# Optimization experiments

Hardware: AMD Instinct MI355X
Metric: run time of the kernel (lower is better)

Reference implementation:

```python
import jax, jax.numpy as jnp
import numpy as np

B, L, D, N_ORIG, GD, K_TARGET = 8, 512, 1024, 8192, 64, 256
_PI, _PJ = np.triu_indices(L, k=1)  # all global pairs i<j, shared across batch


def setup_inputs() -> dict:
    key = jax.random.key(0)
    k1, k2, k3 = jax.random.split(key, 3)
    x = jax.random.normal(k1, (B, L, D), jnp.float32)
    source = jax.random.uniform(k2, (B, L, N_ORIG), jnp.float32)
    W = jax.random.normal(k3, (GD, D), jnp.float32) * 0.02  # group_proj weight (out,in), no bias
    return {"x": x, "source": source, "W": W, "target_len": K_TARGET}


def _merge_single(x, s, W, r_step, pi, pj):
    # x: (S,D), s: (S,N). One greedy global merge step (r_step = S//2 >= r_total).
    S = x.shape[0]
    g = x @ W.T                                   # (S, GD)
    gn = jnp.linalg.norm(g, axis=-1)              # token weights (g.norm)
    gu = g / jnp.maximum(gn, 1e-12)[:, None]      # F.normalize(g, dim=-1)
    sim = (gu[pi] * gu[pj]).sum(-1)               # (P,) cosine sim of each pair
    # deterministic order: (-sim, i, j); lexsort's last key is primary
    order = jnp.lexsort((pj, pi, -sim))
    si = pi[order]
    sj = pj[order]

    # sequential greedy disjoint (mutual-exclusion) selection
    def body(carry, ij):
        partner, isj, cnt = carry
        i, j = ij
        used_i = (partner[i] >= 0) | isj[i]
        used_j = (partner[j] >= 0) | isj[j]
        sel = (~used_i) & (~used_j) & (cnt < r_step)
        partner = partner.at[i].set(jnp.where(sel, j, partner[i]))
        isj = isj.at[j].set(isj[j] | sel)
        return (partner, isj, cnt + sel.astype(jnp.int32)), None

    init = (jnp.full((S,), -1, jnp.int32), jnp.zeros((S,), bool), jnp.int32(0))
    (partner, isj, _), _ = jax.lax.scan(body, init, (si, sj))

    # kept tokens (everything not a merged-away j), in original order; greedy on a
    # complete graph always selects exactly r_step pairs, so K = S - r_step is static
    K = S - r_step
    keep = jnp.argsort(isj.astype(jnp.int32), stable=True)[:K]  # (K,)
    pk = partner[keep]
    has_p = pk >= 0
    pjx = jnp.where(has_p, pk, keep)  # safe partner index
    wi = gn[keep]
    wj = gn[pjx]
    tot = wi + wj + 1e-8
    xm = jnp.where(has_p[:, None], (wi[:, None] * x[keep] + wj[:, None] * x[pjx]) / tot[:, None], x[keep])
    sm = jnp.where(has_p[:, None], s[keep] + s[pjx], s[keep])
    return xm, sm


def reference(x, source, W, target_len):
    Bb, Ll, Dd = x.shape
    r_total = Ll - target_len
    if r_total <= 0:
        return x, source
    # with target_len = L//2, r_total <= floor(L/2): single greedy step (faithful)
    r_step = min(r_total, Ll // 2)
    pi = jnp.asarray(_PI, jnp.int32)
    pj = jnp.asarray(_PJ, jnp.int32)
    f = lambda xb, sb: _merge_single(xb, sb, W, r_step, pi, pj)
    return jax.vmap(f)(x, source)
```

## Files before the change

kernel.cpp:

```cpp
#include <hip/hip_runtime.h>

#define B_ 8
#define L_ 512
#define D_ 1024
#define N_ 8192
#define GD_ 64
#define K_ 256
#define CD_ 24

#define XQ(q) ((q) ^ (((q) >> 4) & 7))

__global__ __launch_bounds__(256) void wt_kernel(const float* __restrict__ W,
                                                 float* __restrict__ Wt) {
  int idx = blockIdx.x * 256 + threadIdx.x;
  int d = idx >> 6, g = idx & 63;
  Wt[idx] = W[(size_t)g * D_ + d];
}

__global__ __launch_bounds__(256) void gproj_kernel(const float* __restrict__ x,
                                                    const float* __restrict__ Wt,
                                                    float* __restrict__ gu,
                                                    float* __restrict__ gn) {
  __shared__ __align__(16) float xs[16 * 1024];
  __shared__ __align__(16) float red[16][16][64];
  int blk = blockIdx.x;
  int b = blk >> 5;
  int t0 = (blk & 31) * 16;
  int tid = threadIdx.x;
  const float* xb = x + ((size_t)b * L_ + t0) * D_;
  for (int r = 0; r < 16; ++r) {
    int idx = r * 256 + tid;
    int tok = idx >> 8, q = idx & 255;
    float4 v = *(const float4*)(xb + (size_t)tok * D_ + q * 4);
    *(float4*)&xs[tok * 1024 + XQ(q) * 4] = v;
  }
  __syncthreads();
  int dq = tid & 15, kg = tid >> 4;
  float acc[16][4];
#pragma unroll
  for (int t = 0; t < 16; ++t)
#pragma unroll
    for (int d = 0; d < 4; ++d) acc[t][d] = 0.f;
  const float* wbase = Wt + (size_t)(kg * 64) * GD_ + dq * 4;
#pragma unroll 1
  for (int sub = 0; sub < 4; ++sub) {
    float4 wv[16];
#pragma unroll
    for (int kk = 0; kk < 16; ++kk)
      wv[kk] = *(const float4*)(wbase + (size_t)(sub * 16 + kk) * GD_);
#pragma unroll
    for (int tok = 0; tok < 16; ++tok) {
      float4 xv[4];
#pragma unroll
      for (int kq = 0; kq < 4; ++kq) {
        int q = kg * 16 + sub * 4 + kq;
        xv[kq] = *(const float4*)&xs[tok * 1024 + XQ(q) * 4];
      }
#pragma unroll
      for (int kq = 0; kq < 4; ++kq) {
        float xc[4] = {xv[kq].x, xv[kq].y, xv[kq].z, xv[kq].w};
#pragma unroll
        for (int c = 0; c < 4; ++c) {
          float4 w = wv[kq * 4 + c];
          acc[tok][0] += xc[c] * w.x;
          acc[tok][1] += xc[c] * w.y;
          acc[tok][2] += xc[c] * w.z;
          acc[tok][3] += xc[c] * w.w;
        }
      }
    }
  }
#pragma unroll
  for (int tok = 0; tok < 16; ++tok) {
    float4 p;
    p.x = acc[tok][0]; p.y = acc[tok][1]; p.z = acc[tok][2]; p.w = acc[tok][3];
    *(float4*)&red[kg][tok][dq * 4] = p;
  }
  __syncthreads();
  int tok = tid >> 4, dqo = tid & 15;
  float g[4] = {0.f, 0.f, 0.f, 0.f};
#pragma unroll
  for (int k = 0; k < 16; ++k) {
    float4 p = *(const float4*)&red[k][tok][dqo * 4];
    g[0] += p.x; g[1] += p.y; g[2] += p.z; g[3] += p.w;
  }
  double ss = 0.0;
#pragma unroll
  for (int d = 0; d < 4; ++d) ss += (double)g[d] * (double)g[d];
#pragma unroll
  for (int off = 1; off < 16; off <<= 1) ss += __shfl_xor(ss, off);
  float gnv = (float)sqrt(ss);
  float dn = fmaxf(gnv, 1e-12f);
  int t = t0 + tok;
  if (dqo == 0) gn[(size_t)b * L_ + t] = gnv;
  float4 o;
  o.x = g[0] / dn; o.y = g[1] / dn; o.z = g[2] / dn; o.w = g[3] / dn;
  *(float4*)(gu + ((size_t)b * L_ + t) * GD_ + dqo * 4) = o;
}

__global__ __launch_bounds__(256) void sim_topk_kernel(const float* __restrict__ gu,
                                                       float* __restrict__ simo,
                                                       unsigned long long* __restrict__ cand) {
  __shared__ __align__(16) float simL[16][512];
  __shared__ __align__(16) float BsT[64][68];
  int b = blockIdx.y;
  int i0 = blockIdx.x * 16;
  const float* gb = gu + (size_t)b * L_ * GD_;
  int tid = threadIdx.x;
  int r = tid >> 4, c4 = (tid & 15) * 4;
  float af[GD_];
  const float4* arow = (const float4*)(gb + (size_t)(i0 + r) * GD_);
#pragma unroll
  for (int q = 0; q < 16; ++q) *(float4*)&af[q * 4] = arow[q];
  float* sgl = simo + (size_t)b * L_ * L_;
#pragma unroll 1
  for (int jt = 0; jt < 8; ++jt) {
    int j0 = jt * 64;
    for (int f = tid; f < 64 * GD_; f += 256) {
      int br = f >> 6, k = f & 63;
      BsT[k][br] = gb[(size_t)(j0 + br) * GD_ + k];
    }
    __syncthreads();
    double a0 = 0, a1 = 0, a2 = 0, a3 = 0;
#pragma unroll
    for (int k = 0; k < GD_; ++k) {
      double a = (double)af[k];
      float4 bv = *(const float4*)&BsT[k][c4];
      a0 += a * (double)bv.x;
      a1 += a * (double)bv.y;
      a2 += a * (double)bv.z;
      a3 += a * (double)bv.w;
    }
    float4 o;
    o.x = (float)a0; o.y = (float)a1; o.z = (float)a2; o.w = (float)a3;
    *(float4*)&simL[r][j0 + c4] = o;
    *(float4*)(sgl + (size_t)(i0 + r) * L_ + (j0 + c4)) = o;
    __syncthreads();
  }
  int wave = tid >> 6, lane = tid & 63;
  for (int rr = wave; rr < 16; rr += 4) {
    int a = i0 + rr;
    int c0 = lane * 8;
    float vv[8];
#pragma unroll
    for (int s = 0; s < 8; ++s) vv[s] = simL[rr][c0 + s];
    unsigned long long k[8];
#pragma unroll
    for (int s = 0; s < 8; ++s) {
      int bb = c0 + s;
      if (bb == a) {
        k[s] = 0;
      } else {
        unsigned u = __float_as_uint(vv[s]);
        u = (u & 0x80000000u) ? ~u : (u | 0x80000000u);
        int i = a < bb ? a : bb, j = a < bb ? bb : a;
        k[s] = ((unsigned long long)u << 18) |
               (unsigned long long)(0x3FFFFu - (((unsigned)i << 9) | (unsigned)j));
      }
    }
    unsigned long long* out = cand + ((size_t)b * L_ + a) * CD_;
#pragma unroll 1
    for (int pass = 0; pass < CD_; ++pass) {
      unsigned long long m = k[0];
#pragma unroll
      for (int s = 1; s < 8; ++s) m = k[s] > m ? k[s] : m;
#pragma unroll
      for (int off = 32; off; off >>= 1) {
        unsigned long long o = __shfl_xor(m, off);
        if (o > m) m = o;
      }
#pragma unroll
      for (int s = 0; s < 8; ++s)
        if (k[s] == m) k[s] = 0;
      if (lane == 0) out[pass] = m;
    }
  }
}

__global__ __launch_bounds__(512) void match_kernel(const float* __restrict__ sim,
                                                    const unsigned long long* __restrict__ cand,
                                                    int* __restrict__ keepI,
                                                    int* __restrict__ keepJ) {
  int b = blockIdx.x;
  const float* S = sim + (size_t)b * L_ * L_;
  const unsigned long long* C = cand + (size_t)b * L_ * CD_;
  __shared__ unsigned long long candL[L_][CD_];
  __shared__ unsigned long long bestkey[L_];
  __shared__ short partner[L_];
  __shared__ short liveA[L_], liveB[L_], rescanQ[L_];
  __shared__ unsigned char liveF[L_], needs[L_], head[L_];
  __shared__ int cnt[2], nQ[2];
  int tid = threadIdx.x;
  int wave = tid >> 6, lane = tid & 63;
  for (int f = tid; f < L_ * (CD_ / 2); f += 512)
    ((ulonglong2*)candL)[f] = ((const ulonglong2*)C)[f];
  if (tid < L_) {
    partner[tid] = -1;
    liveF[tid] = 1;
    needs[tid] = 1;
    head[tid] = 0;
    liveA[tid] = (short)tid;
    bestkey[tid] = 0ull;
  }
  if (tid == 0) {
    cnt[0] = L_; cnt[1] = 0;
    nQ[0] = 0; nQ[1] = 0;
  }
  __syncthreads();
  for (int round = 0; round < 300; ++round) {
    int par = round & 1;
    int nLive = cnt[par];
    if (nLive == 0) break;
    short* cur = par ? liveB : liveA;
    short* nxt = par ? liveA : liveB;
    if (tid == 0) {
      cnt[par ^ 1] = 0;
      nQ[par ^ 1] = 0;
    }
    for (int idx = tid; idx < nLive; idx += 512) {
      int a = cur[idx];
      if (needs[a]) {
        int h = head[a];
        unsigned long long bk = 0ull;
        while (h < CD_) {
          unsigned long long key = candL[a][h];
          if (key) {
            unsigned pk = 0x3FFFFu - (unsigned)(key & 0x3FFFFull);
            int i = (int)(pk >> 9), j = (int)(pk & 511u);
            int p = (i == a) ? j : i;
            if (liveF[p]) { bk = key; break; }
          }
          ++h;
        }
        head[a] = (unsigned char)h;
        if (bk) {
          bestkey[a] = bk;
          needs[a] = 0;
        } else {
          int q = atomicAdd(&nQ[par], 1);
          rescanQ[q] = (short)a;
        }
      }
    }
    __syncthreads();
    int nq = nQ[par];
    if (nq > 0) {
      for (int q = wave; q < nq; q += 8) {
        int a = rescanQ[q];
        unsigned long long mk = 0ull;
        for (int kk = lane; kk < nLive; kk += 64) {
          int bb = cur[kk];
          if (bb != a) {
            float sv = S[(size_t)a * L_ + bb];
            unsigned u = __float_as_uint(sv);
            u = (u & 0x80000000u) ? ~u : (u | 0x80000000u);
            int i = a < bb ? a : bb, j = a < bb ? bb : a;
            unsigned long long key =
                ((unsigned long long)u << 18) |
                (unsigned long long)(0x3FFFFu - (((unsigned)i << 9) | (unsigned)j));
            if (key > mk) mk = key;
          }
        }
#pragma unroll
        for (int off = 32; off; off >>= 1) {
          unsigned long long o = __shfl_xor(mk, off);
          if (o > mk) mk = o;
        }
        if (lane == 0) {
          bestkey[a] = mk;
          needs[a] = 0;
        }
      }
      __syncthreads();
    }
    for (int idx = tid; idx < nLive; idx += 512) {
      int a = cur[idx];
      unsigned pk = 0x3FFFFu - (unsigned)(bestkey[a] & 0x3FFFFull);
      int i = (int)(pk >> 9), j = (int)(pk & 511u);
      int p = (i == a) ? j : i;
      unsigned pk2 = 0x3FFFFu - (unsigned)(bestkey[p] & 0x3FFFFull);
      int i2 = (int)(pk2 >> 9), j2 = (int)(pk2 & 511u);
      int p2 = (i2 == p) ? j2 : i2;
      if (p2 == a) {
        partner[a] = (short)p;
        liveF[a] = 0;
      }
    }
    __syncthreads();
    for (int idx = tid; idx < nLive; idx += 512) {
      int a = cur[idx];
      if (liveF[a]) {
        unsigned pk = 0x3FFFFu - (unsigned)(bestkey[a] & 0x3FFFFull);
        int i = (int)(pk >> 9), j = (int)(pk & 511u);
        int p = (i == a) ? j : i;
        if (!liveF[p]) needs[a] = 1;
        int pos = atomicAdd(&cnt[par ^ 1], 1);
        nxt[pos] = (short)a;
      }
    }
    __syncthreads();
  }
  if (wave == 0) {
    int base = 0;
    for (int c = 0; c < 8; ++c) {
      int a = c * 64 + lane;
      bool kept = partner[a] > a;
      unsigned long long m = __ballot(kept);
      int pos = base + (int)__popcll(m & ((1ull << lane) - 1ull));
      if (kept) {
        keepI[b * K_ + pos] = a;
        keepJ[b * K_ + pos] = partner[a];
      }
      base += (int)__popcll(m);
    }
  }
}

__global__ __launch_bounds__(256) void merge_kernel(const float* __restrict__ x,
                                                    const float* __restrict__ s,
                                                    const float* __restrict__ gn,
                                                    const int* __restrict__ keepI,
                                                    const int* __restrict__ keepJ,
                                                    float* __restrict__ xm,
                                                    float* __restrict__ sm) {
  int blk = blockIdx.x;
  int row = blk >> 1, half = blk & 1;
  int b = row >> 8;
  int i = keepI[row], j = keepJ[row];
  int t = threadIdx.x;
  if (half == 0) {
    float wi = gn[(size_t)b * L_ + i], wj = gn[(size_t)b * L_ + j];
    float tot = wi + wj + 1e-8f;
    const float4* xi = (const float4*)(x + ((size_t)b * L_ + i) * D_);
    const float4* xj = (const float4*)(x + ((size_t)b * L_ + j) * D_);
    float4* o = (float4*)(xm + (size_t)row * D_);
    float4 a = xi[t], c = xj[t];
    float4 r;
    r.x = (wi * a.x + wj * c.x) / tot;
    r.y = (wi * a.y + wj * c.y) / tot;
    r.z = (wi * a.z + wj * c.z) / tot;
    r.w = (wi * a.w + wj * c.w) / tot;
    o[t] = r;
  }
  {
    size_t off = (size_t)half * (N_ / 2);
    const float4* si = (const float4*)(s + ((size_t)b * L_ + i) * N_ + off);
    const float4* sj = (const float4*)(s + ((size_t)b * L_ + j) * N_ + off);
    float4* o = (float4*)(sm + (size_t)row * N_ + off);
    for (int tt = t; tt < N_ / 8; tt += 256) {
      float4 a = si[tt], c = sj[tt];
      float4 r;
      r.x = a.x + c.x;
      r.y = a.y + c.y;
      r.z = a.z + c.z;
      r.w = a.w + c.w;
      o[tt] = r;
    }
  }
}

extern "C" void kernel_launch(void* const* d_in, const int* in_sizes, int n_in,
                              void* d_out, int out_size, void* d_ws, size_t ws_size,
                              hipStream_t stream) {
  (void)in_sizes; (void)n_in; (void)out_size; (void)ws_size;
  const float* x = (const float*)d_in[0];
  const float* src = (const float*)d_in[1];
  const float* W = (const float*)d_in[2];

  float* ws = (float*)d_ws;
  float* Wt = ws;
  float* gu = Wt + 65536;
  float* gn = gu + (size_t)B_ * L_ * GD_;
  float* sim = gn + (size_t)B_ * L_;
  int* keepI = (int*)(sim + (size_t)B_ * L_ * L_);
  int* keepJ = keepI + B_ * K_;
  unsigned long long* cand = (unsigned long long*)(keepJ + B_ * K_);

  float* xm = (float*)d_out;
  float* sm = xm + (size_t)B_ * K_ * D_;

  wt_kernel<<<256, 256, 0, stream>>>(W, Wt);
  gproj_kernel<<<256, 256, 0, stream>>>(x, Wt, gu, gn);
  sim_topk_kernel<<<dim3(32, 8), 256, 0, stream>>>(gu, sim, cand);
  match_kernel<<<B_, 512, 0, stream>>>(sim, cand, keepI, keepJ);
  merge_kernel<<<B_ * K_ * 2, 256, 0, stream>>>(x, src, gn, keepI, keepJ, xm, sm);
}
```

Before: 358.8 us.

## Split sim/top-k into separate tiled kernels and shrink candidate depth

Splits the fused similarity and top-k kernel into a 2D-tiled sim kernel (2048 blocks of 32x32 tiles) and a separate top-k kernel with one wave per row. The fused version ran only 256 blocks, each looping serially over column tiles. The change also cuts the per-row candidate count from 24 to 16, which shortens the top-k passes and shrinks the candidate list the match kernel loads. The split adds an extra launch and a re-read of the sim matrix from global memory. The smaller candidate depth may also make the match kernel fall back to rescans more often.

```diff
diff --git a/kernel.cpp b/kernel.cpp
--- a/kernel.cpp
+++ b/kernel.cpp
@@ -6,7 +6,7 @@
 #define N_ 8192
 #define GD_ 64
 #define K_ 256
-#define CD_ 24
+#define CD_ 16
 
 #define XQ(q) ((q) ^ (((q) >> 4) & 7))
 
@@ -98,82 +98,78 @@
   *(float4*)(gu + ((size_t)b * L_ + t) * GD_ + dqo * 4) = o;
 }
 
-__global__ __launch_bounds__(256) void sim_topk_kernel(const float* __restrict__ gu,
-                                                       float* __restrict__ simo,
-                                                       unsigned long long* __restrict__ cand) {
-  __shared__ __align__(16) float simL[16][512];
-  __shared__ __align__(16) float BsT[64][68];
-  int b = blockIdx.y;
-  int i0 = blockIdx.x * 16;
+__global__ __launch_bounds__(256) void sim_kernel(const float* __restrict__ gu,
+                                                  float* __restrict__ simo) {
+  __shared__ __align__(16) float BsT[GD_][36];
+  int b = blockIdx.z;
+  int i0 = blockIdx.y * 32, j0 = blockIdx.x * 32;
   const float* gb = gu + (size_t)b * L_ * GD_;
   int tid = threadIdx.x;
-  int r = tid >> 4, c4 = (tid & 15) * 4;
+  for (int f = tid; f < 32 * GD_; f += 256) {
+    int r = f >> 6, k = f & 63;
+    BsT[k][r] = gb[(size_t)(j0 + r) * GD_ + k];
+  }
+  int r = tid >> 3, c4 = (tid & 7) * 4;
   float af[GD_];
   const float4* arow = (const float4*)(gb + (size_t)(i0 + r) * GD_);
 #pragma unroll
   for (int q = 0; q < 16; ++q) *(float4*)&af[q * 4] = arow[q];
-  float* sgl = simo + (size_t)b * L_ * L_;
-#pragma unroll 1
-  for (int jt = 0; jt < 8; ++jt) {
-    int j0 = jt * 64;
-    for (int f = tid; f < 64 * GD_; f += 256) {
-      int br = f >> 6, k = f & 63;
-      BsT[k][br] = gb[(size_t)(j0 + br) * GD_ + k];
-    }
-    __syncthreads();
-    double a0 = 0, a1 = 0, a2 = 0, a3 = 0;
-#pragma unroll
-    for (int k = 0; k < GD_; ++k) {
-      double a = (double)af[k];
-      float4 bv = *(const float4*)&BsT[k][c4];
-      a0 += a * (double)bv.x;
-      a1 += a * (double)bv.y;
-      a2 += a * (double)bv.z;
-      a3 += a * (double)bv.w;
-    }
-    float4 o;
-    o.x = (float)a0; o.y = (float)a1; o.z = (float)a2; o.w = (float)a3;
-    *(float4*)&simL[r][j0 + c4] = o;
-    *(float4*)(sgl + (size_t)(i0 + r) * L_ + (j0 + c4)) = o;
-    __syncthreads();
-  }
-  int wave = tid >> 6, lane = tid & 63;
-  for (int rr = wave; rr < 16; rr += 4) {
-    int a = i0 + rr;
-    int c0 = lane * 8;
-    float vv[8];
-#pragma unroll
-    for (int s = 0; s < 8; ++s) vv[s] = simL[rr][c0 + s];
-    unsigned long long k[8];
-#pragma unroll
-    for (int s = 0; s < 8; ++s) {
-      int bb = c0 + s;
-      if (bb == a) {
-        k[s] = 0;
-      } else {
-        unsigned u = __float_as_uint(vv[s]);
-        u = (u & 0x80000000u) ? ~u : (u | 0x80000000u);
-        int i = a < bb ? a : bb, j = a < bb ? bb : a;
-        k[s] = ((unsigned long long)u << 18) |
-               (unsigned long long)(0x3FFFFu - (((unsigned)i << 9) | (unsigned)j));
-      }
-    }
-    unsigned long long* out = cand + ((size_t)b * L_ + a) * CD_;
-#pragma unroll 1
-    for (int pass = 0; pass < CD_; ++pass) {
-      unsigned long long m = k[0];
-#pragma unroll
-      for (int s = 1; s < 8; ++s) m = k[s] > m ? k[s] : m;
-#pragma unroll
-      for (int off = 32; off; off >>= 1) {
-        unsigned long long o = __shfl_xor(m, off);
-        if (o > m) m = o;
-      }
-#pragma unroll
-      for (int s = 0; s < 8; ++s)
-        if (k[s] == m) k[s] = 0;
-      if (lane == 0) out[pass] = m;
-    }
+  __syncthreads();
+  double a0 = 0, a1 = 0, a2 = 0, a3 = 0;
+#pragma unroll
+  for (int k = 0; k < GD_; ++k) {
+    double a = (double)af[k];
+    float4 bv = *(const float4*)&BsT[k][c4];
+    a0 += a * (double)bv.x;
+    a1 += a * (double)bv.y;
+    a2 += a * (double)bv.z;
+    a3 += a * (double)bv.w;
+  }
+  float4 o;
+  o.x = (float)a0; o.y = (float)a1; o.z = (float)a2; o.w = (float)a3;
+  *(float4*)(simo + (size_t)b * L_ * L_ + (size_t)(i0 + r) * L_ + (j0 + c4)) = o;
+}
+
+__global__ __launch_bounds__(256) void topk_kernel(const float* __restrict__ sim,
+                                                   unsigned long long* __restrict__ cand) {
+  int wid = blockIdx.x * 4 + (threadIdx.x >> 6);
+  int b = wid >> 9;
+  int a = wid & 511;
+  int lane = threadIdx.x & 63;
+  const float* row = sim + ((size_t)b * L_ + a) * L_;
+  int c0 = lane * 8;
+  float4 v0 = *(const float4*)(row + c0);
+  float4 v1 = *(const float4*)(row + c0 + 4);
+  float vv[8] = {v0.x, v0.y, v0.z, v0.w, v1.x, v1.y, v1.z, v1.w};
+  unsigned long long k[8];
+#pragma unroll
+  for (int s = 0; s < 8; ++s) {
+    int bb = c0 + s;
+    if (bb == a) {
+      k[s] = 0;
+    } else {
+      unsigned u = __float_as_uint(vv[s]);
+      u = (u & 0x80000000u) ? ~u : (u | 0x80000000u);
+      int i = a < bb ? a : bb, j = a < bb ? bb : a;
+      k[s] = ((unsigned long long)u << 18) |
+             (unsigned long long)(0x3FFFFu - (((unsigned)i << 9) | (unsigned)j));
+    }
+  }
+  unsigned long long* out = cand + ((size_t)b * L_ + a) * CD_;
+#pragma unroll
+  for (int pass = 0; pass < CD_; ++pass) {
+    unsigned long long m = k[0];
+#pragma unroll
+    for (int s = 1; s < 8; ++s) m = k[s] > m ? k[s] : m;
+#pragma unroll
+    for (int off = 32; off; off >>= 1) {
+      unsigned long long o = __shfl_xor(m, off);
+      if (o > m) m = o;
+    }
+#pragma unroll
+    for (int s = 0; s < 8; ++s)
+      if (k[s] == m) k[s] = 0;
+    if (lane == 0) out[pass] = m;
   }
 }
 
@@ -381,7 +377,8 @@
 
   wt_kernel<<<256, 256, 0, stream>>>(W, Wt);
   gproj_kernel<<<256, 256, 0, stream>>>(x, Wt, gu, gn);
-  sim_topk_kernel<<<dim3(32, 8), 256, 0, stream>>>(gu, sim, cand);
+  sim_kernel<<<dim3(16, 16, 8), 256, 0, stream>>>(gu, sim);
+  topk_kernel<<<1024, 256, 0, stream>>>(sim, cand);
   match_kernel<<<B_, 512, 0, stream>>>(sim, cand, keepI, keepJ);
   merge_kernel<<<B_ * K_ * 2, 256, 0, stream>>>(x, src, gn, keepI, keepJ, xm, sm);
 }
```

Result: faster. 307.7 us (-14.2%).
